# Performance work log

Measured on AMD Instinct MI355X. Metric: run time of the kernel, lower is better.

The kernel has to match this reference:

```python
import jax, jax.numpy as jnp
import numpy as np

N = 4096      # nodes
IN = 512      # in_features
HEADS = 8
HPH = 8       # n_hidden // n_heads
HID = HEADS * HPH  # 64
CLS = 16      # n_classes
NEG_SLOPE = 0.2
MASK_VAL = -1e9


def setup_inputs() -> dict:
    key = jax.random.key(0)
    ks = jax.random.split(key, 8)
    x = jax.random.normal(ks[0], (N, IN), jnp.float32)
    # sparse-ish adjacency, avg degree ~16, with self loops
    adj = jax.random.bernoulli(ks[1], 16.0 / N, (N, N)) | jnp.eye(N, dtype=bool)
    W1 = jax.random.normal(ks[2], (IN, HEADS, HPH), jnp.float32) * 0.05
    a1l = jax.random.normal(ks[3], (HEADS, HPH), jnp.float32) * 0.05
    a1r = jax.random.normal(ks[4], (HEADS, HPH), jnp.float32) * 0.05
    W2 = jax.random.normal(ks[5], (HID, 1, CLS), jnp.float32) * 0.05
    a2l = jax.random.normal(ks[6], (1, CLS), jnp.float32) * 0.05
    a2r = jax.random.normal(ks[7], (1, CLS), jnp.float32) * 0.05
    return {"x": x, "adj": adj, "W1": W1, "a1l": a1l, "a1r": a1r,
            "W2": W2, "a2l": a2l, "a2r": a2r}


def gat_layer(x, adj, W, al, ar, is_concat):
    # project: [N, H, D]
    g = jnp.einsum('ni,ihd->nhd', x, W)
    # score e[i,j,h] = leaky_relu(a_l . g_i + a_r . g_j)
    sl = jnp.einsum('nhd,hd->nh', g, al)  # [N, H]
    sr = jnp.einsum('nhd,hd->nh', g, ar)  # [N, H]
    e = jax.nn.leaky_relu(sl[:, None, :] + sr[None, :, :], NEG_SLOPE)  # [N, N, H]
    e = jnp.where(adj[:, :, None], e, MASK_VAL)
    a = jax.nn.softmax(e, axis=1)                 # softmax over neighbors j
    out = jnp.einsum('ijh,jhd->ihd', a, g)        # [N, H, D]
    if is_concat:
        return out.reshape(out.shape[0], -1)      # [N, H*D]
    return out.mean(axis=1)                        # [N, D]


def reference(x, adj, W1, a1l, a1r, W2, a2l, a2r):
    # dropout layers are identity in eval mode
    h = gat_layer(x, adj, W1, a1l, a1r, True)   # [N, HID]
    h = jax.nn.elu(h)
    return gat_layer(h, adj, W2, a2l, a2r, False)  # [N, CLS]
```

## Files before the change

### kernel.cpp

```cpp
#include <hip/hip_runtime.h>
#include <hip/hip_bf16.h>

#define N_NODES 4096
#define IN_F 512
#define HEADS 8
#define HPH 8
#define HID 64
#define CLS 16
#define NEG_SLOPE 0.2f
#define MAXD 256

__device__ __forceinline__ float leaky(float x) { return x > 0.f ? x : NEG_SLOPE * x; }

__global__ __launch_bounds__(256, 2) void scan_proj1(
        const int* __restrict__ adj,
        const float* __restrict__ x,
        const float* __restrict__ W1,
        const float* __restrict__ a1l,
        const float* __restrict__ a1r,
        float* __restrict__ g1,
        float* __restrict__ sl1,
        float* __restrict__ sr1,
        int* __restrict__ deg_g,
        int* __restrict__ nbr_g) {
    __shared__ float xs[4][516];
    const int b = blockIdx.x;
    const int t = threadIdx.x;
    if ((b & 1) == 0) {
        int* nbrS = (int*)&xs[0][0];
        __shared__ int cntS[4];
        const int w = t >> 6, lane = t & 63;
        if (lane == 0) cntS[w] = 0;
        const int i = (b >> 1) * 4 + w;
        const int4* row = (const int4*)(adj + (size_t)i * N_NODES);
#pragma unroll
        for (int pass = 0; pass < 2; ++pass) {
            int4 v[8];
#pragma unroll
            for (int s = 0; s < 8; ++s) v[s] = row[lane + 64 * (pass * 8 + s)];
#pragma unroll
            for (int s = 0; s < 8; ++s) {
                const int base = 4 * (lane + 64 * (pass * 8 + s));
                if (v[s].x | v[s].y | v[s].z | v[s].w) {
                    if (v[s].x) { int p = atomicAdd(&cntS[w], 1); if (p < MAXD) nbrS[w * MAXD + p] = base; }
                    if (v[s].y) { int p = atomicAdd(&cntS[w], 1); if (p < MAXD) nbrS[w * MAXD + p] = base + 1; }
                    if (v[s].z) { int p = atomicAdd(&cntS[w], 1); if (p < MAXD) nbrS[w * MAXD + p] = base + 2; }
                    if (v[s].w) { int p = atomicAdd(&cntS[w], 1); if (p < MAXD) nbrS[w * MAXD + p] = base + 3; }
                }
            }
        }
        const int n = cntS[w] < MAXD ? cntS[w] : MAXD;
        if (lane == 0) deg_g[i] = n;
        for (int k = lane; k < n; k += 64) nbr_g[(size_t)i * MAXD + k] = nbrS[w * MAXD + k];
        return;
    }
    const int i0 = (b >> 1) * 4;
    const int nl = t >> 6;
    const int inner = t & 63;
    const int kq = inner >> 4;
    const int cg = inner & 15;
    for (int l = t; l < 512; l += 256) {
        const int r = l >> 7, c4 = l & 127;
        *(float4*)&xs[r][c4 * 4] = *(const float4*)(x + (size_t)(i0 + r) * IN_F + c4 * 4);
    }
    __syncthreads();
    float4 acc = make_float4(0.f, 0.f, 0.f, 0.f);
    const float* xrow = &xs[nl][kq * 128];
    const float* Wq = W1 + (size_t)(kq * 128) * HID + cg * 4;
#pragma unroll 4
    for (int k = 0; k < 128; k += 4) {
        const float4 xv = *(const float4*)(xrow + k);
        const float4 w0 = *(const float4*)(Wq + (size_t)(k + 0) * HID);
        const float4 w1 = *(const float4*)(Wq + (size_t)(k + 1) * HID);
        const float4 w2 = *(const float4*)(Wq + (size_t)(k + 2) * HID);
        const float4 w3 = *(const float4*)(Wq + (size_t)(k + 3) * HID);
        acc.x += xv.x * w0.x + xv.y * w1.x + xv.z * w2.x + xv.w * w3.x;
        acc.y += xv.x * w0.y + xv.y * w1.y + xv.z * w2.y + xv.w * w3.y;
        acc.z += xv.x * w0.z + xv.y * w1.z + xv.z * w2.z + xv.w * w3.z;
        acc.w += xv.x * w0.w + xv.y * w1.w + xv.z * w2.w + xv.w * w3.w;
    }
#pragma unroll
    for (int m = 16; m <= 32; m <<= 1) {
        acc.x += __shfl_xor(acc.x, m, 64);
        acc.y += __shfl_xor(acc.y, m, 64);
        acc.z += __shfl_xor(acc.z, m, 64);
        acc.w += __shfl_xor(acc.w, m, 64);
    }
    if (kq == 0) {
        const int i = i0 + nl;
        *(float4*)(g1 + (size_t)i * HID + cg * 4) = acc;
        const float4 al = *(const float4*)(a1l + cg * 4);
        const float4 ar = *(const float4*)(a1r + cg * 4);
        float pl = acc.x * al.x + acc.y * al.y + acc.z * al.z + acc.w * al.w;
        float pr = acc.x * ar.x + acc.y * ar.y + acc.z * ar.z + acc.w * ar.w;
        pl += __shfl_xor(pl, 1, 64);
        pr += __shfl_xor(pr, 1, 64);
        if ((cg & 1) == 0) {
            sl1[i * HEADS + (cg >> 1)] = pl;
            sr1[i * HEADS + (cg >> 1)] = pr;
        }
    }
}

__global__ __launch_bounds__(64) void attn1_fused(
        const float* __restrict__ g1,
        const float* __restrict__ sl1,
        const float* __restrict__ sr1,
        const float* __restrict__ W2,
        const float* __restrict__ a2l,
        const float* __restrict__ a2r,
        const int* __restrict__ deg_g,
        const int* __restrict__ nbr_g,
        float* __restrict__ g2,
        float* __restrict__ sl2,
        float* __restrict__ sr2) {
    const int i = blockIdx.x;
    const int t = threadIdx.x;
    __shared__ int nbr[MAXD];
    __shared__ float h1s[HID];
    const int n = deg_g[i];
    for (int k = t; k < n; k += 64) nbr[k] = nbr_g[(size_t)i * MAXD + k];
    __syncthreads();
    const int h = t >> 3;
    const float sl = sl1[i * HEADS + h];
    float denom = 0.f, acc = 0.f;
    int k = 0;
    for (; k + 4 <= n; k += 4) {
        const int j0 = nbr[k], j1 = nbr[k + 1], j2 = nbr[k + 2], j3 = nbr[k + 3];
        const float s0 = sr1[j0 * HEADS + h], s1 = sr1[j1 * HEADS + h];
        const float s2 = sr1[j2 * HEADS + h], s3 = sr1[j3 * HEADS + h];
        const float v0 = g1[(size_t)j0 * HID + t], v1 = g1[(size_t)j1 * HID + t];
        const float v2 = g1[(size_t)j2 * HID + t], v3 = g1[(size_t)j3 * HID + t];
        const float w0 = __expf(leaky(sl + s0)), w1 = __expf(leaky(sl + s1));
        const float w2 = __expf(leaky(sl + s2)), w3 = __expf(leaky(sl + s3));
        denom += (w0 + w1) + (w2 + w3);
        acc += w0 * v0; acc += w1 * v1; acc += w2 * v2; acc += w3 * v3;
    }
    for (; k < n; ++k) {
        const int jj = nbr[k];
        const float w = __expf(leaky(sl + sr1[jj * HEADS + h]));
        denom += w;
        acc += w * g1[(size_t)jj * HID + t];
    }
    float o = (n > 0) ? (acc / denom) : 0.f;
    o = (o > 0.f) ? o : expm1f(o);
    h1s[t] = o;
    __syncthreads();
    const int q = t >> 4, c = t & 15;
    float p = 0.f;
#pragma unroll
    for (int kk = 0; kk < 16; ++kk) {
        const int k2 = q * 16 + kk;
        p += h1s[k2] * W2[k2 * CLS + c];
    }
    p += __shfl_xor(p, 16, 64);
    p += __shfl_xor(p, 32, 64);
    float pl = 0.f, pr = 0.f;
    if (t < CLS) {
        g2[(size_t)i * CLS + t] = p;
        pl = p * a2l[t];
        pr = p * a2r[t];
    }
#pragma unroll
    for (int off = 1; off < 16; off <<= 1) {
        pl += __shfl_xor(pl, off, 64);
        pr += __shfl_xor(pr, off, 64);
    }
    if (t == 0) { sl2[i] = pl; sr2[i] = pr; }
}

__global__ __launch_bounds__(64) void attn2(
        const int* __restrict__ deg_g,
        const int* __restrict__ nbr_g,
        const float* __restrict__ g2,
        const float* __restrict__ sl2,
        const float* __restrict__ sr2,
        float* __restrict__ out) {
    const int t = threadIdx.x;
    const int g = t >> 4;
    const int c = t & 15;
    const int node = blockIdx.x * 4 + g;
    __shared__ int nbrs[4][MAXD];
    const int n = deg_g[node];
    for (int k = c; k < n; k += 16) nbrs[g][k] = nbr_g[(size_t)node * MAXD + k];
    __syncthreads();
    const float sl = sl2[node];
    float denom = 0.f, acc = 0.f;
    int k = 0;
    for (; k + 4 <= n; k += 4) {
        const int j0 = nbrs[g][k], j1 = nbrs[g][k + 1];
        const int j2 = nbrs[g][k + 2], j3 = nbrs[g][k + 3];
        const float s0 = sr2[j0], s1 = sr2[j1], s2 = sr2[j2], s3 = sr2[j3];
        const float v0 = g2[(size_t)j0 * CLS + c], v1 = g2[(size_t)j1 * CLS + c];
        const float v2 = g2[(size_t)j2 * CLS + c], v3 = g2[(size_t)j3 * CLS + c];
        const float w0 = __expf(leaky(sl + s0)), w1 = __expf(leaky(sl + s1));
        const float w2 = __expf(leaky(sl + s2)), w3 = __expf(leaky(sl + s3));
        denom += (w0 + w1) + (w2 + w3);
        acc += w0 * v0; acc += w1 * v1; acc += w2 * v2; acc += w3 * v3;
    }
    for (; k < n; ++k) {
        const int jj = nbrs[g][k];
        const float w = __expf(leaky(sl + sr2[jj]));
        denom += w;
        acc += w * g2[(size_t)jj * CLS + c];
    }
    out[(size_t)node * CLS + c] = (n > 0) ? acc / denom : 0.f;
}

extern "C" void kernel_launch(void* const* d_in, const int* in_sizes, int n_in,
                              void* d_out, int out_size, void* d_ws, size_t ws_size,
                              hipStream_t stream) {
    const float* x   = (const float*)d_in[0];
    const int*   adj = (const int*)d_in[1];
    const float* W1  = (const float*)d_in[2];
    const float* a1l = (const float*)d_in[3];
    const float* a1r = (const float*)d_in[4];
    const float* W2  = (const float*)d_in[5];
    const float* a2l = (const float*)d_in[6];
    const float* a2r = (const float*)d_in[7];
    float* out = (float*)d_out;

    float* ws  = (float*)d_ws;
    float* g1  = ws;
    float* sl1 = g1  + (size_t)N_NODES * HID;
    float* sr1 = sl1 + (size_t)N_NODES * HEADS;
    float* g2  = sr1 + (size_t)N_NODES * HEADS;
    float* sl2 = g2  + (size_t)N_NODES * CLS;
    float* sr2 = sl2 + N_NODES;
    int*   deg = (int*)(sr2 + N_NODES);
    int*   nbr = deg + N_NODES;

    scan_proj1<<<2 * (N_NODES / 4), 256, 0, stream>>>(
        adj, x, W1, a1l, a1r, g1, sl1, sr1, deg, nbr);
    attn1_fused<<<N_NODES, 64, 0, stream>>>(g1, sl1, sr1, W2, a2l, a2r,
                                            deg, nbr, g2, sl2, sr2);
    attn2<<<N_NODES / 4, 64, 0, stream>>>(deg, nbr, g2, sl2, sr2, out);
}
```

Baseline: 141.4 us.

## Split adjacency scan and layer-1 projection into separate kernels, retile projection

The combined scan/projection kernel, which alternated block roles, becomes two kernels: a pure adjacency scan and a projection kernel. The projection now handles 16 nodes per block, with each thread computing a full 512-long dot product instead of a quarter plus cross-lane reductions. This removes the shuffle reductions and reuses each W1 load across more rows per block. The cost is an extra kernel launch, losing the overlap between the memory-bound scan and the compute-bound projection, and a larger shared-memory footprint (about 33 KB) that may limit occupancy.

```diff
diff --git a/kernel.cpp b/kernel.cpp
--- a/kernel.cpp
+++ b/kernel.cpp
@@ -12,93 +12,80 @@
 
 __device__ __forceinline__ float leaky(float x) { return x > 0.f ? x : NEG_SLOPE * x; }
 
-__global__ __launch_bounds__(256, 2) void scan_proj1(
-        const int* __restrict__ adj,
-        const float* __restrict__ x,
-        const float* __restrict__ W1,
-        const float* __restrict__ a1l,
-        const float* __restrict__ a1r,
-        float* __restrict__ g1,
-        float* __restrict__ sl1,
-        float* __restrict__ sr1,
-        int* __restrict__ deg_g,
-        int* __restrict__ nbr_g) {
-    __shared__ float xs[4][516];
-    const int b = blockIdx.x;
+__global__ __launch_bounds__(256) void scan(const int* __restrict__ adj,
+                                            int* __restrict__ deg_g,
+                                            int* __restrict__ nbr_g) {
+    __shared__ int nbrS[4][MAXD];
+    __shared__ int cntS[4];
     const int t = threadIdx.x;
-    if ((b & 1) == 0) {
-        int* nbrS = (int*)&xs[0][0];
-        __shared__ int cntS[4];
-        const int w = t >> 6, lane = t & 63;
-        if (lane == 0) cntS[w] = 0;
-        const int i = (b >> 1) * 4 + w;
-        const int4* row = (const int4*)(adj + (size_t)i * N_NODES);
-#pragma unroll
-        for (int pass = 0; pass < 2; ++pass) {
-            int4 v[8];
-#pragma unroll
-            for (int s = 0; s < 8; ++s) v[s] = row[lane + 64 * (pass * 8 + s)];
-#pragma unroll
-            for (int s = 0; s < 8; ++s) {
-                const int base = 4 * (lane + 64 * (pass * 8 + s));
-                if (v[s].x | v[s].y | v[s].z | v[s].w) {
-                    if (v[s].x) { int p = atomicAdd(&cntS[w], 1); if (p < MAXD) nbrS[w * MAXD + p] = base; }
-                    if (v[s].y) { int p = atomicAdd(&cntS[w], 1); if (p < MAXD) nbrS[w * MAXD + p] = base + 1; }
-                    if (v[s].z) { int p = atomicAdd(&cntS[w], 1); if (p < MAXD) nbrS[w * MAXD + p] = base + 2; }
-                    if (v[s].w) { int p = atomicAdd(&cntS[w], 1); if (p < MAXD) nbrS[w * MAXD + p] = base + 3; }
-                }
+    const int w = t >> 6, lane = t & 63;
+    if (lane == 0) cntS[w] = 0;
+    const int i = blockIdx.x * 4 + w;
+    const int4* row = (const int4*)(adj + (size_t)i * N_NODES);
+#pragma unroll
+    for (int pass = 0; pass < 2; ++pass) {
+        int4 v[8];
+#pragma unroll
+        for (int s = 0; s < 8; ++s) v[s] = row[lane + 64 * (pass * 8 + s)];
+#pragma unroll
+        for (int s = 0; s < 8; ++s) {
+            const int base = 4 * (lane + 64 * (pass * 8 + s));
+            if (v[s].x | v[s].y | v[s].z | v[s].w) {
+                if (v[s].x) { int p = atomicAdd(&cntS[w], 1); if (p < MAXD) nbrS[w][p] = base; }
+                if (v[s].y) { int p = atomicAdd(&cntS[w], 1); if (p < MAXD) nbrS[w][p] = base + 1; }
+                if (v[s].z) { int p = atomicAdd(&cntS[w], 1); if (p < MAXD) nbrS[w][p] = base + 2; }
+                if (v[s].w) { int p = atomicAdd(&cntS[w], 1); if (p < MAXD) nbrS[w][p] = base + 3; }
             }
         }
-        const int n = cntS[w] < MAXD ? cntS[w] : MAXD;
-        if (lane == 0) deg_g[i] = n;
-        for (int k = lane; k < n; k += 64) nbr_g[(size_t)i * MAXD + k] = nbrS[w * MAXD + k];
-        return;
-    }
-    const int i0 = (b >> 1) * 4;
-    const int nl = t >> 6;
-    const int inner = t & 63;
-    const int kq = inner >> 4;
-    const int cg = inner & 15;
-    for (int l = t; l < 512; l += 256) {
+    }
+    const int n = cntS[w] < MAXD ? cntS[w] : MAXD;
+    if (lane == 0) deg_g[i] = n;
+    for (int k = lane; k < n; k += 64) nbr_g[(size_t)i * MAXD + k] = nbrS[w][k];
+}
+
+__global__ __launch_bounds__(256, 2) void proj1(const float* __restrict__ x,
+                                                const float* __restrict__ W1,
+                                                const float* __restrict__ a1l,
+                                                const float* __restrict__ a1r,
+                                                float* __restrict__ g1,
+                                                float* __restrict__ sl1,
+                                                float* __restrict__ sr1) {
+    const int t  = threadIdx.x;
+    const int nl = t >> 4;
+    const int cg = t & 15;
+    const int i0 = blockIdx.x * 16;
+    __shared__ float xs[16][516];
+    for (int l = t; l < 16 * IN_F / 4; l += 256) {
         const int r = l >> 7, c4 = l & 127;
         *(float4*)&xs[r][c4 * 4] = *(const float4*)(x + (size_t)(i0 + r) * IN_F + c4 * 4);
     }
     __syncthreads();
     float4 acc = make_float4(0.f, 0.f, 0.f, 0.f);
-    const float* xrow = &xs[nl][kq * 128];
-    const float* Wq = W1 + (size_t)(kq * 128) * HID + cg * 4;
+    const float* xrow = &xs[nl][0];
+    const float* Wc = W1 + cg * 4;
 #pragma unroll 4
-    for (int k = 0; k < 128; k += 4) {
+    for (int k = 0; k < IN_F; k += 4) {
         const float4 xv = *(const float4*)(xrow + k);
-        const float4 w0 = *(const float4*)(Wq + (size_t)(k + 0) * HID);
-        const float4 w1 = *(const float4*)(Wq + (size_t)(k + 1) * HID);
-        const float4 w2 = *(const float4*)(Wq + (size_t)(k + 2) * HID);
-        const float4 w3 = *(const float4*)(Wq + (size_t)(k + 3) * HID);
+        const float4 w0 = *(const float4*)(Wc + (size_t)(k + 0) * HID);
+        const float4 w1 = *(const float4*)(Wc + (size_t)(k + 1) * HID);
+        const float4 w2 = *(const float4*)(Wc + (size_t)(k + 2) * HID);
+        const float4 w3 = *(const float4*)(Wc + (size_t)(k + 3) * HID);
         acc.x += xv.x * w0.x + xv.y * w1.x + xv.z * w2.x + xv.w * w3.x;
         acc.y += xv.x * w0.y + xv.y * w1.y + xv.z * w2.y + xv.w * w3.y;
         acc.z += xv.x * w0.z + xv.y * w1.z + xv.z * w2.z + xv.w * w3.z;
         acc.w += xv.x * w0.w + xv.y * w1.w + xv.z * w2.w + xv.w * w3.w;
     }
-#pragma unroll
-    for (int m = 16; m <= 32; m <<= 1) {
-        acc.x += __shfl_xor(acc.x, m, 64);
-        acc.y += __shfl_xor(acc.y, m, 64);
-        acc.z += __shfl_xor(acc.z, m, 64);
-        acc.w += __shfl_xor(acc.w, m, 64);
-    }
-    if (kq == 0) {
-        const int i = i0 + nl;
-        *(float4*)(g1 + (size_t)i * HID + cg * 4) = acc;
-        const float4 al = *(const float4*)(a1l + cg * 4);
-        const float4 ar = *(const float4*)(a1r + cg * 4);
-        float pl = acc.x * al.x + acc.y * al.y + acc.z * al.z + acc.w * al.w;
-        float pr = acc.x * ar.x + acc.y * ar.y + acc.z * ar.z + acc.w * ar.w;
-        pl += __shfl_xor(pl, 1, 64);
-        pr += __shfl_xor(pr, 1, 64);
-        if ((cg & 1) == 0) {
-            sl1[i * HEADS + (cg >> 1)] = pl;
-            sr1[i * HEADS + (cg >> 1)] = pr;
-        }
+    const int i = i0 + nl;
+    *(float4*)(g1 + (size_t)i * HID + cg * 4) = acc;
+    const float4 al = *(const float4*)(a1l + cg * 4);
+    const float4 ar = *(const float4*)(a1r + cg * 4);
+    float pl = acc.x * al.x + acc.y * al.y + acc.z * al.z + acc.w * al.w;
+    float pr = acc.x * ar.x + acc.y * ar.y + acc.z * ar.z + acc.w * ar.w;
+    pl += __shfl_xor(pl, 1, 64);
+    pr += __shfl_xor(pr, 1, 64);
+    if ((cg & 1) == 0) {
+        sl1[i * HEADS + (cg >> 1)] = pl;
+        sr1[i * HEADS + (cg >> 1)] = pr;
     }
 }
 
@@ -230,8 +217,8 @@
     int*   deg = (int*)(sr2 + N_NODES);
     int*   nbr = deg + N_NODES;
 
-    scan_proj1<<<2 * (N_NODES / 4), 256, 0, stream>>>(
-        adj, x, W1, a1l, a1r, g1, sl1, sr1, deg, nbr);
+    scan<<<N_NODES / 4, 256, 0, stream>>>(adj, deg, nbr);
+    proj1<<<N_NODES / 16, 256, 0, stream>>>(x, W1, a1l, a1r, g1, sl1, sr1);
     attn1_fused<<<N_NODES, 64, 0, stream>>>(g1, sl1, sr1, W2, a2l, a2r,
                                             deg, nbr, g2, sl2, sr2);
     attn2<<<N_NODES / 4, 64, 0, stream>>>(deg, nbr, g2, sl2, sr2, out);
```

New measurement: 138.6 us. 1.02x faster.
